# Kernel optimization log

Measured on AMD Instinct MI355X. Metric: run time of the kernel, lower is better.

Reference implementation:

```python
import jax, jax.numpy as jnp
import numpy as np
from jax import lax

KERNEL = 3
SAMPLING_RATE = 100.0
N_GRID = 201  # np.linspace(-1, 1, 201) sub-sample grid


def setup_inputs() -> dict:
    key = jax.random.key(0)
    nb, nc, nx, nt = 32, 3, 64, 4096
    xcorr = jax.random.normal(key, (nb, nc, nx, nt), dtype=jnp.float32)
    return {"xcorr": xcorr, "nlag": nt // 2}


def reference(xcorr, nlag):
    nt = xcorr.shape[-1]
    x = jnp.abs(xcorr)  # vabs=True

    # max_pool2d with (1, kernel=3), stride 1, padding (0, 1) -> SAME max over lag axis
    smax = lax.reduce_window(
        x, -jnp.inf, lax.max,
        window_dimensions=(1, 1, 1, KERNEL),
        window_strides=(1, 1, 1, 1),
        padding=[(0, 0), (0, 0), (0, 0), (KERNEL // 2, KERNEL // 2)],
    )
    keep = (smax == x).astype(x.dtype)

    # top-2 local maxima along lag axis (sorted descending, like torch.topk)
    topk_score, topk_idx = lax.top_k(x * keep, 2)
    s0 = topk_score[..., 0]
    s1 = topk_score[..., 1]
    weight = (0.1 + 3.0 * (s0 - s1)) * s0 ** 2
    i0 = topk_idx[..., 0]  # [nb, nc, nx]

    # --- sub-sample interpolation: 3-point spline == parabola through neighbors ---
    offsets = jnp.array([-1, 0, 1], dtype=i0.dtype)
    nbr_idx = jnp.clip(i0[..., None] + offsets, 0, nt - 1)      # [nb,nc,nx,3]
    y = jnp.take_along_axis(x, nbr_idx, axis=-1)                 # [nb,nc,nx,3]
    ym1, y0, yp1 = y[..., 0], y[..., 1], y[..., 2]
    a = 0.5 * (ym1 + yp1) - y0   # quadratic coeff
    b = 0.5 * (yp1 - ym1)        # linear coeff
    c = y0                       # constant

    xg = jnp.linspace(-1.0, 1.0, N_GRID, dtype=x.dtype)          # [201]
    yg = (a[..., None] * xg + b[..., None]) * xg + c[..., None]  # [nb,nc,nx,201]
    ii = jnp.argmax(yg, axis=-1)                                  # [nb,nc,nx]
    sub_shift = xg[ii]
    topk_idx_f = i0.astype(x.dtype) + sub_shift
    topk_score0 = jnp.take_along_axis(yg, ii[..., None], axis=-1)[..., 0]

    # pick the channel with the largest weight
    idx = jnp.argmax(weight, axis=1, keepdims=True)               # [nb,1,nx]
    max_cc = jnp.take_along_axis(topk_score0, idx, axis=1)
    w = jnp.take_along_axis(weight, idx, axis=1)
    shift_idx = jnp.take_along_axis(topk_idx_f, idx, axis=1) - jnp.asarray(nlag, x.dtype)
    shift_t = shift_idx / SAMPLING_RATE

    # stacked: [cc_max, cc_weight, cc_dt, cc_shift], each [nb,1,nx]
    return jnp.stack([max_cc, w, shift_t, shift_idx], axis=0)
```

## Files before the change

### kernel.cpp

```cpp
#include <hip/hip_runtime.h>
#include <math.h>

#define NB 32
#define NC 3
#define NX 64
#define NT 4096
#define CH_STRIDE ((size_t)NX * NT)

struct Quad { float4 a, b, c, d; };

__device__ __forceinline__ Quad load_row(const float* __restrict__ xr, int wid, int lane) {
    const float* base = xr + (size_t)(wid << 10) + (size_t)(lane << 2);
    Quad q;
    q.a = *reinterpret_cast<const float4*>(base);
    q.b = *reinterpret_cast<const float4*>(base + 256);
    q.c = *reinterpret_cast<const float4*>(base + 512);
    q.d = *reinterpret_cast<const float4*>(base + 768);
    return q;
}

__device__ __forceinline__ void proc4(float a0, float a1, float a2, float a3,
                                      float cl, float cr, int t4,
                                      float& v0, int& i0, float& v1)
{
    const float c0 = (a0 >= cl && a0 >= a1) ? a0 : 0.0f;
    const float c1 = (a1 >= a0 && a1 >= a2) ? a1 : 0.0f;
    const float c2 = (a2 >= a1 && a2 >= a3) ? a2 : 0.0f;
    const float c3 = (a3 >= a2 && a3 >= cr) ? a3 : 0.0f;
    bool g;
    g = c0 > v0; v1 = g ? v0 : fmaxf(v1, c0); v0 = fmaxf(v0, c0); i0 = g ? t4     : i0;
    g = c1 > v0; v1 = g ? v0 : fmaxf(v1, c1); v0 = fmaxf(v0, c1); i0 = g ? t4 + 1 : i0;
    g = c2 > v0; v1 = g ? v0 : fmaxf(v1, c2); v0 = fmaxf(v0, c2); i0 = g ? t4 + 2 : i0;
    g = c3 > v0; v1 = g ? v0 : fmaxf(v1, c3); v0 = fmaxf(v0, c3); i0 = g ? t4 + 3 : i0;
}

__device__ __forceinline__ void scan_row(Quad q, float lmf, float rmf,
                                         int wid, int lane,
                                         float& v0, int& i0, float& v1)
{
    const int base = (wid << 10) + (lane << 2);
    v0 = -1.0f; v1 = -1.0f; i0 = 0;

    const float a00 = fabsf(q.a.x), a01 = fabsf(q.a.y), a02 = fabsf(q.a.z), a03 = fabsf(q.a.w);
    const float a10 = fabsf(q.b.x), a11 = fabsf(q.b.y), a12 = fabsf(q.b.z), a13 = fabsf(q.b.w);
    const float a20 = fabsf(q.c.x), a21 = fabsf(q.c.y), a22 = fabsf(q.c.z), a23 = fabsf(q.c.w);
    const float a30 = fabsf(q.d.x), a31 = fabsf(q.d.y), a32 = fabsf(q.d.z), a33 = fabsf(q.d.w);

    float lm, rm, t;

    lm = __shfl_up(a03, 1);
    lm = (lane == 0) ? ((wid > 0) ? lmf : -INFINITY) : lm;
    rm = __shfl_down(a00, 1);
    t  = __shfl(a10, 0);
    rm = (lane == 63) ? t : rm;
    proc4(a00, a01, a02, a03, lm, rm, base, v0, i0, v1);

    lm = __shfl_up(a13, 1);
    t  = __shfl(a03, 63);
    lm = (lane == 0) ? t : lm;
    rm = __shfl_down(a10, 1);
    t  = __shfl(a20, 0);
    rm = (lane == 63) ? t : rm;
    proc4(a10, a11, a12, a13, lm, rm, base + 256, v0, i0, v1);

    lm = __shfl_up(a23, 1);
    t  = __shfl(a13, 63);
    lm = (lane == 0) ? t : lm;
    rm = __shfl_down(a20, 1);
    t  = __shfl(a30, 0);
    rm = (lane == 63) ? t : rm;
    proc4(a20, a21, a22, a23, lm, rm, base + 512, v0, i0, v1);

    lm = __shfl_up(a33, 1);
    t  = __shfl(a23, 63);
    lm = (lane == 0) ? t : lm;
    rm = __shfl_down(a30, 1);
    rm = (lane == 63) ? ((wid < 3) ? rmf : -INFINITY) : rm;
    proc4(a30, a31, a32, a33, lm, rm, base + 768, v0, i0, v1);

    #pragma unroll
    for (int off = 1; off < 64; off <<= 1) {
        const float ov0 = __shfl_xor(v0, off);
        const int   oi0 = __shfl_xor(i0, off);
        const float ov1 = __shfl_xor(v1, off);
        const bool big = (ov0 > v0) || (ov0 == v0 && oi0 < i0);
        const float loser = big ? v0 : ov0;
        v1 = fmaxf(fmaxf(v1, ov1), loser);
        v0 = big ? ov0 : v0;
        i0 = big ? oi0 : i0;
    }
}

__device__ __forceinline__ void merge4(const float sv0c[4], const int si0c[4],
                                       const float sv1c[4],
                                       float& m0, int& mi, float& m1)
{
    m0 = sv0c[0]; mi = si0c[0]; m1 = sv1c[0];
    #pragma unroll
    for (int w = 1; w < 4; ++w) {
        const float b0 = sv0c[w]; const int bi = si0c[w]; const float b1 = sv1c[w];
        const bool big = (b0 > m0) || (b0 == m0 && bi < mi);
        const float loser = big ? m0 : b0;
        m1 = fmaxf(fmaxf(m1, b1), loser);
        m0 = big ? b0 : m0;
        mi = big ? bi : mi;
    }
}

__global__ __launch_bounds__(256) void detect_peaks_kernel(
    const float* __restrict__ xcorr,
    const int*   __restrict__ nlag_p,
    float* __restrict__ out)
{
    __shared__ float sv0[NC][4], sv1[NC][4];
    __shared__ int   si0[NC][4];

    const int bid  = blockIdx.x;
    const int b    = bid >> 6;
    const int x    = bid & 63;
    const int tid  = threadIdx.x;
    const int lane = tid & 63;
    const int wid  = tid >> 6;

    const float* __restrict__ xr0 = xcorr + ((size_t)(b * NC) * NX + x) * NT;
    const float* __restrict__ xr1 = xr0 + CH_STRIDE;
    const float* __restrict__ xr2 = xr0 + 2 * CH_STRIDE;

    Quad q0 = load_row(xr0, wid, lane);
    Quad q1 = load_row(xr1, wid, lane);
    Quad q2 = load_row(xr2, wid, lane);

    const int liE = (wid > 0) ? (wid << 10) - 1    : 0;
    const int riE = (wid < 3) ? (wid << 10) + 1024 : NT - 1;
    const float l0 = fabsf(xr0[liE]), r0 = fabsf(xr0[riE]);
    const float l1 = fabsf(xr1[liE]), r1 = fabsf(xr1[riE]);
    const float l2 = fabsf(xr2[liE]), r2 = fabsf(xr2[riE]);

    float v0, v1; int i0;

    scan_row(q0, l0, r0, wid, lane, v0, i0, v1);
    if (lane == 0) { sv0[0][wid] = v0; si0[0][wid] = i0; sv1[0][wid] = v1; }

    scan_row(q1, l1, r1, wid, lane, v0, i0, v1);
    if (lane == 0) { sv0[1][wid] = v0; si0[1][wid] = i0; sv1[1][wid] = v1; }

    scan_row(q2, l2, r2, wid, lane, v0, i0, v1);
    if (lane == 0) { sv0[2][wid] = v0; si0[2][wid] = i0; sv1[2][wid] = v1; }

    __syncthreads();

    float m00, m01, m02, m10, m11, m12; int p0, p1, p2;
    merge4(sv0[0], si0[0], sv1[0], m00, p0, m10);
    merge4(sv0[1], si0[1], sv1[1], m01, p1, m11);
    merge4(sv0[2], si0[2], sv1[2], m02, p2, m12);

    const float w0 = (0.1f + 3.0f * (m00 - m10)) * (m00 * m00);
    const float w1 = (0.1f + 3.0f * (m01 - m11)) * (m01 * m01);
    const float w2 = (0.1f + 3.0f * (m02 - m12)) * (m02 * m02);

    const bool t1 = w1 > w0;
    float bw = t1 ? w1 : w0;
    float bs = t1 ? m01 : m00;
    int   bp = t1 ? p1 : p0;
    const float* xrs = t1 ? xr1 : xr0;
    const bool t2 = w2 > bw;
    bw  = t2 ? w2 : bw;
    bs  = t2 ? m02 : bs;
    bp  = t2 ? p2 : bp;
    xrs = t2 ? xr2 : xrs;

    if (tid == 0) {
        const float ym1 = fabsf(xrs[bp > 0 ? bp - 1 : 0]);
        const float yp1 = fabsf(xrs[bp < NT - 1 ? bp + 1 : NT - 1]);
        const float A = 0.5f * (ym1 + yp1) - bs;
        const float B = 0.5f * (yp1 - ym1);
        const float C = bs;

        int gi; float bv;
        if (A == 0.0f) {
            gi = (B > 0.0f) ? 200 : 0;
            const float xg = 0.01f * (float)(gi - 100);
            bv = (A * xg + B) * xg + C;
        } else {
            float gv = (1.0f - 0.5f * B / A) * 100.0f;
            gv = fminf(fmaxf(gv, 0.0f), 200.0f);
            const int glo = (int)gv;
            bv = -INFINITY; gi = 0;
            #pragma unroll
            for (int d = -1; d <= 2; ++d) {
                int g = glo + d;
                g = g < 0 ? 0 : (g > 200 ? 200 : g);
                const float xg = 0.01f * (float)(g - 100);
                const float yg = (A * xg + B) * xg + C;
                if (yg > bv) { bv = yg; gi = g; }
            }
        }

        const float fidx = (float)bp + 0.01f * (float)(gi - 100);
        const float nlagf = (float)(*nlag_p);
        const float shift_idx = fidx - nlagf;
        const int n = NB * NX;
        const int o = b * NX + x;
        out[0 * n + o] = bv;
        out[1 * n + o] = bw;
        out[2 * n + o] = shift_idx / 100.0f;
        out[3 * n + o] = shift_idx;
    }
}

extern "C" void kernel_launch(void* const* d_in, const int* in_sizes, int n_in,
                              void* d_out, int out_size, void* d_ws, size_t ws_size,
                              hipStream_t stream) {
    const float* xcorr  = (const float*)d_in[0];
    const int*   nlag_p = (const int*)d_in[1];
    float* out = (float*)d_out;

    detect_peaks_kernel<<<NB * NX, 256, 0, stream>>>(xcorr, nlag_p, out);
}
```

Measured before the change: 25.08 us.

## Process two (b,x) tiles per block with software-pipelined loads

Each block now handles two output positions instead of one, halving the grid to 1024 blocks. The loads for the second tile are issued early and interleaved with scanning of the first tile, so memory latency overlaps with compute. This raises register pressure from holding six Quads, and reduces the number of blocks available to hide latency across the GPU.

After: 28.17 us. 1.12x slower.

```diff
diff --git a/kernel.cpp b/kernel.cpp
--- a/kernel.cpp
+++ b/kernel.cpp
@@ -107,52 +107,17 @@
     }
 }
 
-__global__ __launch_bounds__(256) void detect_peaks_kernel(
-    const float* __restrict__ xcorr,
-    const int*   __restrict__ nlag_p,
-    float* __restrict__ out)
-{
-    __shared__ float sv0[NC][4], sv1[NC][4];
-    __shared__ int   si0[NC][4];
-
-    const int bid  = blockIdx.x;
-    const int b    = bid >> 6;
-    const int x    = bid & 63;
-    const int tid  = threadIdx.x;
-    const int lane = tid & 63;
-    const int wid  = tid >> 6;
-
-    const float* __restrict__ xr0 = xcorr + ((size_t)(b * NC) * NX + x) * NT;
-    const float* __restrict__ xr1 = xr0 + CH_STRIDE;
-    const float* __restrict__ xr2 = xr0 + 2 * CH_STRIDE;
-
-    Quad q0 = load_row(xr0, wid, lane);
-    Quad q1 = load_row(xr1, wid, lane);
-    Quad q2 = load_row(xr2, wid, lane);
-
-    const int liE = (wid > 0) ? (wid << 10) - 1    : 0;
-    const int riE = (wid < 3) ? (wid << 10) + 1024 : NT - 1;
-    const float l0 = fabsf(xr0[liE]), r0 = fabsf(xr0[riE]);
-    const float l1 = fabsf(xr1[liE]), r1 = fabsf(xr1[riE]);
-    const float l2 = fabsf(xr2[liE]), r2 = fabsf(xr2[riE]);
-
-    float v0, v1; int i0;
-
-    scan_row(q0, l0, r0, wid, lane, v0, i0, v1);
-    if (lane == 0) { sv0[0][wid] = v0; si0[0][wid] = i0; sv1[0][wid] = v1; }
-
-    scan_row(q1, l1, r1, wid, lane, v0, i0, v1);
-    if (lane == 0) { sv0[1][wid] = v0; si0[1][wid] = i0; sv1[1][wid] = v1; }
-
-    scan_row(q2, l2, r2, wid, lane, v0, i0, v1);
-    if (lane == 0) { sv0[2][wid] = v0; si0[2][wid] = i0; sv1[2][wid] = v1; }
-
-    __syncthreads();
-
+__device__ __forceinline__ void tile_epilogue(
+    const float sv0s[NC][4], const int si0s[NC][4], const float sv1s[NC][4],
+    const float* __restrict__ xr0, const float* __restrict__ xr1,
+    const float* __restrict__ xr2,
+    const int* __restrict__ nlag_p, float* __restrict__ out,
+    int g, int tid)
+{
     float m00, m01, m02, m10, m11, m12; int p0, p1, p2;
-    merge4(sv0[0], si0[0], sv1[0], m00, p0, m10);
-    merge4(sv0[1], si0[1], sv1[1], m01, p1, m11);
-    merge4(sv0[2], si0[2], sv1[2], m02, p2, m12);
+    merge4(sv0s[0], si0s[0], sv1s[0], m00, p0, m10);
+    merge4(sv0s[1], si0s[1], sv1s[1], m01, p1, m11);
+    merge4(sv0s[2], si0s[2], sv1s[2], m02, p2, m12);
 
     const float w0 = (0.1f + 3.0f * (m00 - m10)) * (m00 * m00);
     const float w1 = (0.1f + 3.0f * (m01 - m11)) * (m01 * m01);
@@ -188,11 +153,11 @@
             bv = -INFINITY; gi = 0;
             #pragma unroll
             for (int d = -1; d <= 2; ++d) {
-                int g = glo + d;
-                g = g < 0 ? 0 : (g > 200 ? 200 : g);
-                const float xg = 0.01f * (float)(g - 100);
+                int gg = glo + d;
+                gg = gg < 0 ? 0 : (gg > 200 ? 200 : gg);
+                const float xg = 0.01f * (float)(gg - 100);
                 const float yg = (A * xg + B) * xg + C;
-                if (yg > bv) { bv = yg; gi = g; }
+                if (yg > bv) { bv = yg; gi = gg; }
             }
         }
 
@@ -200,12 +165,79 @@
         const float nlagf = (float)(*nlag_p);
         const float shift_idx = fidx - nlagf;
         const int n = NB * NX;
-        const int o = b * NX + x;
-        out[0 * n + o] = bv;
-        out[1 * n + o] = bw;
-        out[2 * n + o] = shift_idx / 100.0f;
-        out[3 * n + o] = shift_idx;
+        out[0 * n + g] = bv;
+        out[1 * n + g] = bw;
+        out[2 * n + g] = shift_idx / 100.0f;
+        out[3 * n + g] = shift_idx;
     }
+}
+
+__global__ __launch_bounds__(256) void detect_peaks_kernel(
+    const float* __restrict__ xcorr,
+    const int*   __restrict__ nlag_p,
+    float* __restrict__ out)
+{
+    __shared__ float sv0[2][NC][4], sv1[2][NC][4];
+    __shared__ int   si0[2][NC][4];
+
+    const int bid  = blockIdx.x;
+    const int tid  = threadIdx.x;
+    const int lane = tid & 63;
+    const int wid  = tid >> 6;
+
+    const int gA = 2 * bid;
+    const int gB = 2 * bid + 1;
+
+    const float* __restrict__ xA0 = xcorr + ((size_t)((gA >> 6) * NC) * NX + (gA & 63)) * NT;
+    const float* __restrict__ xA1 = xA0 + CH_STRIDE;
+    const float* __restrict__ xA2 = xA0 + 2 * CH_STRIDE;
+    const float* __restrict__ xB0 = xcorr + ((size_t)((gB >> 6) * NC) * NX + (gB & 63)) * NT;
+    const float* __restrict__ xB1 = xB0 + CH_STRIDE;
+    const float* __restrict__ xB2 = xB0 + 2 * CH_STRIDE;
+
+    const int liE = (wid > 0) ? (wid << 10) - 1    : 0;
+    const int riE = (wid < 3) ? (wid << 10) + 1024 : NT - 1;
+
+    Quad qA0 = load_row(xA0, wid, lane);
+    Quad qA1 = load_row(xA1, wid, lane);
+    Quad qA2 = load_row(xA2, wid, lane);
+    const float lA0 = xA0[liE], rA0 = xA0[riE];
+    const float lA1 = xA1[liE], rA1 = xA1[riE];
+    const float lA2 = xA2[liE], rA2 = xA2[riE];
+    Quad qB0 = load_row(xB0, wid, lane);
+    const float lB0 = xB0[liE], rB0 = xB0[riE];
+    const float lB1 = xB1[liE], rB1 = xB1[riE];
+    const float lB2 = xB2[liE], rB2 = xB2[riE];
+
+    float v0, v1; int i0;
+
+    scan_row(qA0, fabsf(lA0), fabsf(rA0), wid, lane, v0, i0, v1);
+    Quad qB1 = load_row(xB1, wid, lane);
+    if (lane == 0) { sv0[0][0][wid] = v0; si0[0][0][wid] = i0; sv1[0][0][wid] = v1; }
+
+    scan_row(qA1, fabsf(lA1), fabsf(rA1), wid, lane, v0, i0, v1);
+    Quad qB2 = load_row(xB2, wid, lane);
+    if (lane == 0) { sv0[0][1][wid] = v0; si0[0][1][wid] = i0; sv1[0][1][wid] = v1; }
+
+    scan_row(qA2, fabsf(lA2), fabsf(rA2), wid, lane, v0, i0, v1);
+    if (lane == 0) { sv0[0][2][wid] = v0; si0[0][2][wid] = i0; sv1[0][2][wid] = v1; }
+
+    __syncthreads();
+
+    tile_epilogue(sv0[0], si0[0], sv1[0], xA0, xA1, xA2, nlag_p, out, gA, tid);
+
+    scan_row(qB0, fabsf(lB0), fabsf(rB0), wid, lane, v0, i0, v1);
+    if (lane == 0) { sv0[1][0][wid] = v0; si0[1][0][wid] = i0; sv1[1][0][wid] = v1; }
+
+    scan_row(qB1, fabsf(lB1), fabsf(rB1), wid, lane, v0, i0, v1);
+    if (lane == 0) { sv0[1][1][wid] = v0; si0[1][1][wid] = i0; sv1[1][1][wid] = v1; }
+
+    scan_row(qB2, fabsf(lB2), fabsf(rB2), wid, lane, v0, i0, v1);
+    if (lane == 0) { sv0[1][2][wid] = v0; si0[1][2][wid] = i0; sv1[1][2][wid] = v1; }
+
+    __syncthreads();
+
+    tile_epilogue(sv0[1], si0[1], sv1[1], xB0, xB1, xB2, nlag_p, out, gB, tid);
 }
 
 extern "C" void kernel_launch(void* const* d_in, const int* in_sizes, int n_in,
@@ -215,5 +247,5 @@
     const int*   nlag_p = (const int*)d_in[1];
     float* out = (float*)d_out;
 
-    detect_peaks_kernel<<<NB * NX, 256, 0, stream>>>(xcorr, nlag_p, out);
-}
+    detect_peaks_kernel<<<(NB * NX) / 2, 256, 0, stream>>>(xcorr, nlag_p, out);
+}
```

## Split peak detection into per-row scan kernel and separate epilogue kernel

Applied to the files above, without the earlier changes.

The single kernel, which handled all three channels of one (batch, x) pair per block, is replaced by two kernels. The first launches one block per row, giving three times as many blocks with fewer registers each, and writes per-row top-2 results to workspace. A second small kernel picks the channel by weight, does the parabolic refinement and writes the outputs. This raises parallelism and occupancy for the memory-bound scan, at the cost of an extra launch and a round trip through workspace.

Result: no change. 24.69 us (-1.5%).

```diff
diff --git a/kernel.cpp b/kernel.cpp
--- a/kernel.cpp
+++ b/kernel.cpp
@@ -5,7 +5,7 @@
 #define NC 3
 #define NX 64
 #define NT 4096
-#define CH_STRIDE ((size_t)NX * NT)
+#define NROWS (NB * NC * NX)
 
 struct Quad { float4 a, b, c, d; };
 
@@ -107,52 +107,60 @@
     }
 }
 
-__global__ __launch_bounds__(256) void detect_peaks_kernel(
+__global__ __launch_bounds__(256) void scan_rows_kernel(
     const float* __restrict__ xcorr,
-    const int*   __restrict__ nlag_p,
-    float* __restrict__ out)
-{
-    __shared__ float sv0[NC][4], sv1[NC][4];
-    __shared__ int   si0[NC][4];
-
-    const int bid  = blockIdx.x;
-    const int b    = bid >> 6;
-    const int x    = bid & 63;
+    float* __restrict__ wsv0, int* __restrict__ wsi0, float* __restrict__ wsv1)
+{
+    __shared__ float sv0[4], sv1[4];
+    __shared__ int   si0[4];
+
+    const int row  = blockIdx.x;
     const int tid  = threadIdx.x;
     const int lane = tid & 63;
     const int wid  = tid >> 6;
 
-    const float* __restrict__ xr0 = xcorr + ((size_t)(b * NC) * NX + x) * NT;
-    const float* __restrict__ xr1 = xr0 + CH_STRIDE;
-    const float* __restrict__ xr2 = xr0 + 2 * CH_STRIDE;
-
-    Quad q0 = load_row(xr0, wid, lane);
-    Quad q1 = load_row(xr1, wid, lane);
-    Quad q2 = load_row(xr2, wid, lane);
-
+    const float* __restrict__ xr = xcorr + (size_t)row * NT;
+
+    Quad q = load_row(xr, wid, lane);
     const int liE = (wid > 0) ? (wid << 10) - 1    : 0;
     const int riE = (wid < 3) ? (wid << 10) + 1024 : NT - 1;
-    const float l0 = fabsf(xr0[liE]), r0 = fabsf(xr0[riE]);
-    const float l1 = fabsf(xr1[liE]), r1 = fabsf(xr1[riE]);
-    const float l2 = fabsf(xr2[liE]), r2 = fabsf(xr2[riE]);
+    const float lm = fabsf(xr[liE]);
+    const float rm = fabsf(xr[riE]);
 
     float v0, v1; int i0;
-
-    scan_row(q0, l0, r0, wid, lane, v0, i0, v1);
-    if (lane == 0) { sv0[0][wid] = v0; si0[0][wid] = i0; sv1[0][wid] = v1; }
-
-    scan_row(q1, l1, r1, wid, lane, v0, i0, v1);
-    if (lane == 0) { sv0[1][wid] = v0; si0[1][wid] = i0; sv1[1][wid] = v1; }
-
-    scan_row(q2, l2, r2, wid, lane, v0, i0, v1);
-    if (lane == 0) { sv0[2][wid] = v0; si0[2][wid] = i0; sv1[2][wid] = v1; }
-
+    scan_row(q, lm, rm, wid, lane, v0, i0, v1);
+
+    if (lane == 0) { sv0[wid] = v0; si0[wid] = i0; sv1[wid] = v1; }
     __syncthreads();
 
-    float m00, m01, m02, m10, m11, m12; int p0, p1, p2;
-    merge4(sv0[0], si0[0], sv1[0], m00, p0, m10);
-    merge4(sv0[1], si0[1], sv1[1], m01, p1, m11);
-    merge4(sv0[2], si0[2], sv1[2], m02, p2, m12);
+    if (tid == 0) {
+        float m0, m1; int mi;
+        merge4(sv0, si0, sv1, m0, mi, m1);
+        wsv0[row] = m0;
+        wsi0[row] = mi;
+        wsv1[row] = m1;
+    }
+}
+
+__global__ __launch_bounds__(256) void epilogue_kernel(
+    const float* __restrict__ xcorr,
+    const float* __restrict__ wsv0, const int* __restrict__ wsi0,
+    const float* __restrict__ wsv1,
+    const int*   __restrict__ nlag_p,
+    float* __restrict__ out)
+{
+    const int g = blockIdx.x * 256 + threadIdx.x;
+    if (g >= NB * NX) return;
+    const int b = g >> 6;
+    const int x = g & 63;
+
+    const int r0 = (b * NC + 0) * NX + x;
+    const int r1 = (b * NC + 1) * NX + x;
+    const int r2 = (b * NC + 2) * NX + x;
+
+    const float m00 = wsv0[r0], m10 = wsv1[r0]; const int p0 = wsi0[r0];
+    const float m01 = wsv0[r1], m11 = wsv1[r1]; const int p1 = wsi0[r1];
+    const float m02 = wsv0[r2], m12 = wsv1[r2]; const int p2 = wsi0[r2];
 
     const float w0 = (0.1f + 3.0f * (m00 - m10)) * (m00 * m00);
     const float w1 = (0.1f + 3.0f * (m01 - m11)) * (m01 * m01);
@@ -162,50 +170,49 @@
     float bw = t1 ? w1 : w0;
     float bs = t1 ? m01 : m00;
     int   bp = t1 ? p1 : p0;
-    const float* xrs = t1 ? xr1 : xr0;
+    int   rs = t1 ? r1 : r0;
     const bool t2 = w2 > bw;
-    bw  = t2 ? w2 : bw;
-    bs  = t2 ? m02 : bs;
-    bp  = t2 ? p2 : bp;
-    xrs = t2 ? xr2 : xrs;
-
-    if (tid == 0) {
-        const float ym1 = fabsf(xrs[bp > 0 ? bp - 1 : 0]);
-        const float yp1 = fabsf(xrs[bp < NT - 1 ? bp + 1 : NT - 1]);
-        const float A = 0.5f * (ym1 + yp1) - bs;
-        const float B = 0.5f * (yp1 - ym1);
-        const float C = bs;
-
-        int gi; float bv;
-        if (A == 0.0f) {
-            gi = (B > 0.0f) ? 200 : 0;
-            const float xg = 0.01f * (float)(gi - 100);
-            bv = (A * xg + B) * xg + C;
-        } else {
-            float gv = (1.0f - 0.5f * B / A) * 100.0f;
-            gv = fminf(fmaxf(gv, 0.0f), 200.0f);
-            const int glo = (int)gv;
-            bv = -INFINITY; gi = 0;
-            #pragma unroll
-            for (int d = -1; d <= 2; ++d) {
-                int g = glo + d;
-                g = g < 0 ? 0 : (g > 200 ? 200 : g);
-                const float xg = 0.01f * (float)(g - 100);
-                const float yg = (A * xg + B) * xg + C;
-                if (yg > bv) { bv = yg; gi = g; }
-            }
+    bw = t2 ? w2 : bw;
+    bs = t2 ? m02 : bs;
+    bp = t2 ? p2 : bp;
+    rs = t2 ? r2 : rs;
+
+    const float* __restrict__ xrs = xcorr + (size_t)rs * NT;
+
+    const float ym1 = fabsf(xrs[bp > 0 ? bp - 1 : 0]);
+    const float yp1 = fabsf(xrs[bp < NT - 1 ? bp + 1 : NT - 1]);
+    const float A = 0.5f * (ym1 + yp1) - bs;
+    const float B = 0.5f * (yp1 - ym1);
+    const float C = bs;
+
+    int gi; float bv;
+    if (A == 0.0f) {
+        gi = (B > 0.0f) ? 200 : 0;
+        const float xg = 0.01f * (float)(gi - 100);
+        bv = (A * xg + B) * xg + C;
+    } else {
+        float gv = (1.0f - 0.5f * B / A) * 100.0f;
+        gv = fminf(fmaxf(gv, 0.0f), 200.0f);
+        const int glo = (int)gv;
+        bv = -INFINITY; gi = 0;
+        #pragma unroll
+        for (int d = -1; d <= 2; ++d) {
+            int gg = glo + d;
+            gg = gg < 0 ? 0 : (gg > 200 ? 200 : gg);
+            const float xg = 0.01f * (float)(gg - 100);
+            const float yg = (A * xg + B) * xg + C;
+            if (yg > bv) { bv = yg; gi = gg; }
         }
-
-        const float fidx = (float)bp + 0.01f * (float)(gi - 100);
-        const float nlagf = (float)(*nlag_p);
-        const float shift_idx = fidx - nlagf;
-        const int n = NB * NX;
-        const int o = b * NX + x;
-        out[0 * n + o] = bv;
-        out[1 * n + o] = bw;
-        out[2 * n + o] = shift_idx / 100.0f;
-        out[3 * n + o] = shift_idx;
-    }
+    }
+
+    const float fidx = (float)bp + 0.01f * (float)(gi - 100);
+    const float nlagf = (float)(*nlag_p);
+    const float shift_idx = fidx - nlagf;
+    const int n = NB * NX;
+    out[0 * n + g] = bv;
+    out[1 * n + g] = bw;
+    out[2 * n + g] = shift_idx / 100.0f;
+    out[3 * n + g] = shift_idx;
 }
 
 extern "C" void kernel_launch(void* const* d_in, const int* in_sizes, int n_in,
@@ -215,5 +222,13 @@
     const int*   nlag_p = (const int*)d_in[1];
     float* out = (float*)d_out;
 
-    detect_peaks_kernel<<<NB * NX, 256, 0, stream>>>(xcorr, nlag_p, out);
-}
+    float* ws   = (float*)d_ws;
+    float* wsv0 = ws;
+    int*   wsi0 = (int*)(ws + NROWS);
+    float* wsv1 = ws + 2 * NROWS;
+
+    scan_rows_kernel<<<NROWS, 256, 0, stream>>>(xcorr, wsv0, wsi0, wsv1);
+
+    epilogue_kernel<<<(NB * NX + 255) / 256, 256, 0, stream>>>(
+        xcorr, wsv0, wsi0, wsv1, nlag_p, out);
+}
```
